# Kernel optimization log

Measured on AMD Instinct MI355X. Metric: run time of the kernel, lower is better.

The kernel has to match this reference:

```python
import jax, jax.numpy as jnp
import numpy as np

U = 359347   # user_num (hardcoded in source)
I = 292589   # item_num (hardcoded in source)
D = 64       # factor_num
NNZ = 4_000_000
B = 32768
LAM = 0.001  # lamada


def setup_inputs() -> dict:
    key = jax.random.key(0)
    ks = jax.random.split(key, 19)
    return {
        "ui_rows": jax.random.randint(ks[0], (NNZ,), 0, U, dtype=jnp.int32),
        "ui_cols": jax.random.randint(ks[1], (NNZ,), 0, I, dtype=jnp.int32),
        "ui_vals": jax.random.uniform(ks[2], (NNZ,), dtype=jnp.float32),
        "iu_vals": jax.random.uniform(ks[3], (NNZ,), dtype=jnp.float32),
        "d_i": jax.random.uniform(ks[4], (U,), dtype=jnp.float32),
        "d_j": jax.random.uniform(ks[5], (I,), dtype=jnp.float32),
        "embed_user": jax.random.normal(ks[6], (U, D), dtype=jnp.float32) * 0.01,
        "embed_item": jax.random.normal(ks[7], (I, D), dtype=jnp.float32) * 0.01,
        "add_w": jax.random.normal(ks[8], (1, 3), dtype=jnp.float32),
        "fw1": jax.random.normal(ks[9], (2 * D, D), dtype=jnp.float32) * (1.0 / np.sqrt(D)),
        "fb1": jax.random.normal(ks[10], (2 * D,), dtype=jnp.float32) * 0.01,
        "fw2": jax.random.normal(ks[11], (D, 2 * D), dtype=jnp.float32) * (1.0 / np.sqrt(2 * D)),
        "fb2": jax.random.normal(ks[12], (D,), dtype=jnp.float32) * 0.01,
        "user_bias": jax.random.normal(ks[13], (U, 1), dtype=jnp.float32) * 0.01,
        "item_bias": jax.random.normal(ks[14], (I, 1), dtype=jnp.float32) * 0.01,
        "avg_rating": jax.random.uniform(ks[15], (1,), dtype=jnp.float32) * 5.0,
        "user0": jax.random.randint(ks[16], (B,), 0, U, dtype=jnp.int32),
        "item_i0": jax.random.randint(ks[17], (B,), 0, I, dtype=jnp.int32),
        "ratings": jax.random.uniform(ks[18], (B,), dtype=jnp.float32) * 5.0,
    }


def _spmm(rows, cols, vals, x, num_rows):
    # sparse [num_rows, *] COO @ dense x : gather rows of x by col index,
    # scale by edge value, scatter-add into destination rows.
    return jax.ops.segment_sum(vals[:, None] * x[cols], rows, num_segments=num_rows)


def _leaky(x):
    return jnp.where(x > 0, x, 0.1 * x)


def _user_filter(x, fw1, fb1, fw2, fb2):
    h = _leaky(x @ fw1.T + fb1)
    return _leaky(h @ fw2.T + fb2)


def reference(ui_rows, ui_cols, ui_vals, iu_vals, d_i, d_j,
              embed_user, embed_item, add_w, fw1, fb1, fw2, fb2,
              user_bias, item_bias, avg_rating, user0, item_i0, ratings):
    ue, ie = embed_user, embed_item
    # layer 1: SpMM + degree-scaled residual + ReLU
    g1_u = jax.nn.relu(_spmm(ui_rows, ui_cols, ui_vals, ie, U) + ue * d_i[:, None])
    g1_i = jax.nn.relu(_spmm(ui_cols, ui_rows, iu_vals, ue, I) + ie * d_j[:, None])
    # layer 2
    g2_u = jax.nn.relu(_spmm(ui_rows, ui_cols, ui_vals, g1_i, U) + g1_u * d_i[:, None])
    g2_i = jax.nn.relu(_spmm(ui_cols, ui_rows, iu_vals, g1_u, I) + g1_i * d_j[:, None])
    # learned combination of the 3 layers: Linear(3,1) over the stacked axis
    w = add_w[0]  # [3]
    gcn_u = w[0] * ue + w[1] * g1_u + w[2] * g2_u   # [U, D]
    gcn_i = w[0] * ie + w[1] * g1_i + w[2] * g2_i   # [I, D]
    # batch lookup + shared filter MLP
    user = _user_filter(gcn_u[user0], fw1, fb1, fw2, fb2)      # [B, D]
    item = _user_filter(gcn_i[item_i0], fw1, fb1, fw2, fb2)    # [B, D]
    pred = (user * item).sum(-1) + user_bias[user0, 0] + item_bias[item_i0, 0] + avg_rating
    l2 = LAM * jnp.mean(gcn_u ** 2) + LAM * jnp.mean(gcn_i ** 2)
    loss2 = jnp.mean((pred - ratings) ** 2)
    return loss2 + l2
```

## Files before the change

### kernel.cpp

```cpp
#include <hip/hip_runtime.h>

#define U_NUM 359347
#define I_NUM 292589
#define DDIM  64
#define NNZ_N 4000000
#define BATCH 32768
#define LAM_F 0.001f
#define ACC_SLOTS 2048

#define EPB   4096
#define NBLK  ((NNZ_N + EPB - 1) / EPB)
#define NB_U  ((U_NUM + 1023) >> 10)
#define NB_I  ((I_NUM + 1023) >> 10)

__device__ __forceinline__ float leaky(float x) { return x > 0.f ? x : 0.1f * x; }

__device__ __forceinline__ unsigned short f2bf(float f) {
    unsigned b = __float_as_uint(f);
    b = (b + 0x7FFF + ((b >> 16) & 1)) >> 16;
    return (unsigned short)b;
}
__device__ __forceinline__ float bf2f(unsigned short u) {
    return __uint_as_float((unsigned)u << 16);
}
__device__ __forceinline__ float bflo(unsigned u) { return __uint_as_float(u << 16); }
__device__ __forceinline__ float bfhi(unsigned u) { return __uint_as_float(u & 0xffff0000u); }

__global__ __launch_bounds__(256) void f2bf_k(
    const float4* __restrict__ in, ushort4* __restrict__ out, size_t n4)
{
    size_t stride = (size_t)gridDim.x * 256;
    for (size_t i = (size_t)blockIdx.x * 256 + threadIdx.x; i < n4; i += stride) {
        float4 v = in[i];
        ushort4 o;
        o.x = f2bf(v.x); o.y = f2bf(v.y); o.z = f2bf(v.z); o.w = f2bf(v.w);
        out[i] = o;
    }
}

__global__ __launch_bounds__(256) void l1hist_k(
    const int* __restrict__ keys, int* __restrict__ gh, int nb)
{
    __shared__ int h[512];
    for (int i = threadIdx.x; i < nb; i += 256) h[i] = 0;
    __syncthreads();
    int base = blockIdx.x * EPB;
    int end = min(base + EPB, NNZ_N);
    for (int e = base + threadIdx.x; e < end; e += 256)
        atomicAdd(&h[keys[e] >> 10], 1);
    __syncthreads();
    for (int i = threadIdx.x; i < nb; i += 256)
        gh[i * NBLK + blockIdx.x] = h[i];
}

__global__ __launch_bounds__(256) void scan1_k(int* __restrict__ a, int n, int* __restrict__ bsum)
{
    __shared__ int s[256];
    int t = threadIdx.x;
    int base = blockIdx.x * 1024 + t * 4;
    int v[4];
#pragma unroll
    for (int j = 0; j < 4; ++j) v[j] = (base + j < n) ? a[base + j] : 0;
    s[t] = v[0] + v[1] + v[2] + v[3];
    __syncthreads();
    for (int off = 1; off < 256; off <<= 1) {
        int x = (t >= off) ? s[t - off] : 0;
        __syncthreads();
        s[t] += x;
        __syncthreads();
    }
    if (t == 255) bsum[blockIdx.x] = s[255];
    int run = (t > 0) ? s[t - 1] : 0;
#pragma unroll
    for (int j = 0; j < 4; ++j) {
        if (base + j < n) a[base + j] = run;
        run += v[j];
    }
}

__global__ __launch_bounds__(512) void scan2_k(int* __restrict__ bsum, int nb)
{
    __shared__ int s[512];
    int t = threadIdx.x;
    int v = (t < nb) ? bsum[t] : 0;
    s[t] = v;
    __syncthreads();
    for (int off = 1; off < 512; off <<= 1) {
        int x = (t >= off) ? s[t - off] : 0;
        __syncthreads();
        s[t] += x;
        __syncthreads();
    }
    if (t < nb) bsum[t] = s[t] - v;
}

__global__ __launch_bounds__(256) void scan3_k(int* __restrict__ a, int n,
                                               const int* __restrict__ bsum)
{
    int add = bsum[blockIdx.x];
    int base = blockIdx.x * 1024 + threadIdx.x * 4;
#pragma unroll
    for (int j = 0; j < 4; ++j)
        if (base + j < n) a[base + j] += add;
}

__global__ __launch_bounds__(256) void l1scatter_k(
    const int* __restrict__ keys, const int* __restrict__ gh, int nb,
    int2* __restrict__ out)
{
    __shared__ int cur[512];
    for (int i = threadIdx.x; i < nb; i += 256) cur[i] = gh[i * NBLK + blockIdx.x];
    __syncthreads();
    int base = blockIdx.x * EPB;
    int end = min(base + EPB, NNZ_N);
    for (int e = base + threadIdx.x; e < end; e += 256) {
        int k = keys[e];
        int pos = atomicAdd(&cur[k >> 10], 1);
        out[pos] = make_int2(k, e);
    }
}

__global__ __launch_bounds__(256) void l2sort_k(
    const int2* __restrict__ tmp, const int* __restrict__ gh, int nb,
    const int* __restrict__ colArr, const float* __restrict__ valArr,
    int* __restrict__ ptr, int nrows, int2* __restrict__ ent)
{
    __shared__ int hist[1024];
    __shared__ int ssc[256];
    int b = blockIdx.x;
    int t = threadIdx.x;
    int bucket_base = gh[b * NBLK];
    int bucket_end  = (b == nb - 1) ? NNZ_N : gh[(b + 1) * NBLK];
    for (int i = t; i < 1024; i += 256) hist[i] = 0;
    __syncthreads();
    for (int e = bucket_base + t; e < bucket_end; e += 256)
        atomicAdd(&hist[tmp[e].x & 1023], 1);
    __syncthreads();
    int v0 = hist[t * 4], v1 = hist[t * 4 + 1], v2 = hist[t * 4 + 2], v3 = hist[t * 4 + 3];
    ssc[t] = v0 + v1 + v2 + v3;
    __syncthreads();
    for (int off = 1; off < 256; off <<= 1) {
        int x = (t >= off) ? ssc[t - off] : 0;
        __syncthreads();
        ssc[t] += x;
        __syncthreads();
    }
    int run = (t > 0) ? ssc[t - 1] : 0;
    int g0 = run, g1 = run + v0, g2 = g1 + v1, g3 = g2 + v2;
    hist[t * 4] = g0; hist[t * 4 + 1] = g1; hist[t * 4 + 2] = g2; hist[t * 4 + 3] = g3;
    int rbase = b << 10;
    if (rbase + t * 4 < nrows)     ptr[rbase + t * 4]     = bucket_base + g0;
    if (rbase + t * 4 + 1 < nrows) ptr[rbase + t * 4 + 1] = bucket_base + g1;
    if (rbase + t * 4 + 2 < nrows) ptr[rbase + t * 4 + 2] = bucket_base + g2;
    if (rbase + t * 4 + 3 < nrows) ptr[rbase + t * 4 + 3] = bucket_base + g3;
    if (b == nb - 1 && t == 0) ptr[nrows] = NNZ_N;
    __syncthreads();
    for (int e = bucket_base + t; e < bucket_end; e += 256) {
        int2 q = tmp[e];
        int pos = bucket_base + atomicAdd(&hist[q.x & 1023], 1);
        ent[pos] = make_int2(colArr[q.y], __float_as_int(valArr[q.y]));
    }
}

template <int MODE>
__global__ __launch_bounds__(256) void spmm_csr_k(
    const int* __restrict__ ptr, const int2* __restrict__ ent,
    const unsigned short* __restrict__ x, const unsigned short* base,
    const float* __restrict__ deg, unsigned short* out, int nrows,
    const unsigned short* __restrict__ embed, const float* __restrict__ add_w,
    float* __restrict__ accArr)
{
    int wv = threadIdx.x >> 6, lane = threadIdx.x & 63;
    int r = blockIdx.x * 4 + wv;
    __shared__ float ssum[4];
    if (r < nrows) {
        int s0 = __builtin_amdgcn_readfirstlane(ptr[r]);
        int e0 = __builtin_amdgcn_readfirstlane(ptr[r + 1]);
        float a0 = 0.f, a1 = 0.f, a2 = 0.f, a3 = 0.f;
        int k = s0;
        for (; k + 4 <= e0; k += 4) {
            int2 q0 = ent[k], q1 = ent[k + 1], q2 = ent[k + 2], q3 = ent[k + 3];
            float x0 = bf2f(x[(size_t)q0.x * DDIM + lane]);
            float x1 = bf2f(x[(size_t)q1.x * DDIM + lane]);
            float x2 = bf2f(x[(size_t)q2.x * DDIM + lane]);
            float x3 = bf2f(x[(size_t)q3.x * DDIM + lane]);
            a0 = fmaf(__int_as_float(q0.y), x0, a0);
            a1 = fmaf(__int_as_float(q1.y), x1, a1);
            a2 = fmaf(__int_as_float(q2.y), x2, a2);
            a3 = fmaf(__int_as_float(q3.y), x3, a3);
        }
        for (; k < e0; ++k) {
            int2 q = ent[k];
            a0 = fmaf(__int_as_float(q.y), bf2f(x[(size_t)q.x * DDIM + lane]), a0);
        }
        float acc = (a0 + a1) + (a2 + a3);
        float bb = bf2f(base[(size_t)r * DDIM + lane]);
        float o = fmaxf(fmaf(bb, deg[r], acc), 0.f);
        if (MODE == 0) {
            out[(size_t)r * DDIM + lane] = f2bf(o);
        } else {
            float g = fmaf(add_w[0], bf2f(embed[(size_t)r * DDIM + lane]),
                           fmaf(add_w[1], bb, add_w[2] * o));
            out[(size_t)r * DDIM + lane] = f2bf(g);
            float sq = g * g;
            for (int off = 32; off; off >>= 1) sq += __shfl_down(sq, off);
            if (lane == 0) ssum[wv] = sq;
        }
    } else if (MODE == 1) {
        if (lane == 0) ssum[wv] = 0.f;
    }
    if (MODE == 1) {
        __syncthreads();
        if (threadIdx.x == 0)
            atomicAdd(&accArr[blockIdx.x & (ACC_SLOTS - 1)],
                      ssum[0] + ssum[1] + ssum[2] + ssum[3]);
    }
}

__global__ __launch_bounds__(256) void mlp_k(
    const int* __restrict__ user0, const int* __restrict__ item0,
    const unsigned short* __restrict__ gcnU, const unsigned short* __restrict__ gcnI,
    const float* __restrict__ fw1, const float* __restrict__ fb1,
    const float* __restrict__ fw2, const float* __restrict__ fb2,
    unsigned short* __restrict__ ou, unsigned short* __restrict__ oi)
{
    __shared__ unsigned short xs[64][72];
    __shared__ unsigned short w1s[128][68];
    __shared__ unsigned short w2s[64][140];
    __shared__ unsigned short hs[128][72];
    __shared__ float b1s[128];
    __shared__ float b2s[64];

    int t = threadIdx.x;
    int side = blockIdx.x >> 9;
    int tile = blockIdx.x & 511;
    const int* sel = side ? item0 : user0;
    const unsigned short* gcn = side ? gcnI : gcnU;
    unsigned short* outp = side ? oi : ou;

    {
        int r = t >> 2, c = t & 3;
        int idx = sel[tile * 64 + r];
        const ushort4* src = (const ushort4*)(gcn + (size_t)idx * 64 + c * 16);
        ushort4 v0 = src[0], v1 = src[1], v2 = src[2], v3 = src[3];
        int k0 = c * 16;
        xs[k0 +  0][r] = v0.x; xs[k0 +  1][r] = v0.y; xs[k0 +  2][r] = v0.z; xs[k0 +  3][r] = v0.w;
        xs[k0 +  4][r] = v1.x; xs[k0 +  5][r] = v1.y; xs[k0 +  6][r] = v1.z; xs[k0 +  7][r] = v1.w;
        xs[k0 +  8][r] = v2.x; xs[k0 +  9][r] = v2.y; xs[k0 + 10][r] = v2.z; xs[k0 + 11][r] = v2.w;
        xs[k0 + 12][r] = v3.x; xs[k0 + 13][r] = v3.y; xs[k0 + 14][r] = v3.z; xs[k0 + 15][r] = v3.w;
    }
#pragma unroll
    for (int i = 0; i < 8; ++i) {
        int flat = i * 1024 + t * 4;
        float4 w = *(const float4*)(fw1 + flat);
        int o = flat >> 6, k = flat & 63;
        *(unsigned*)&w1s[o][k]     = (unsigned)f2bf(w.x) | ((unsigned)f2bf(w.y) << 16);
        *(unsigned*)&w1s[o][k + 2] = (unsigned)f2bf(w.z) | ((unsigned)f2bf(w.w) << 16);
        float4 u = *(const float4*)(fw2 + flat);
        int o2 = flat >> 7, k2 = flat & 127;
        *(unsigned*)&w2s[o2][k2]     = (unsigned)f2bf(u.x) | ((unsigned)f2bf(u.y) << 16);
        *(unsigned*)&w2s[o2][k2 + 2] = (unsigned)f2bf(u.z) | ((unsigned)f2bf(u.w) << 16);
    }
    if (t < 128) b1s[t] = fb1[t];
    if (t < 64)  b2s[t] = fb2[t];
    __syncthreads();

    int sg = t & 15, og = t >> 4;

    float acc[4][8];
#pragma unroll
    for (int i = 0; i < 4; ++i)
#pragma unroll
        for (int j = 0; j < 8; ++j) acc[i][j] = 0.f;

    for (int kc = 0; kc < 64; kc += 4) {
        uint2 xp0 = *(const uint2*)&xs[kc    ][sg * 4];
        uint2 xp1 = *(const uint2*)&xs[kc + 1][sg * 4];
        uint2 xp2 = *(const uint2*)&xs[kc + 2][sg * 4];
        uint2 xp3 = *(const uint2*)&xs[kc + 3][sg * 4];
        float x0[4] = { bflo(xp0.x), bfhi(xp0.x), bflo(xp0.y), bfhi(xp0.y) };
        float x1[4] = { bflo(xp1.x), bfhi(xp1.x), bflo(xp1.y), bfhi(xp1.y) };
        float x2[4] = { bflo(xp2.x), bfhi(xp2.x), bflo(xp2.y), bfhi(xp2.y) };
        float x3[4] = { bflo(xp3.x), bfhi(xp3.x), bflo(xp3.y), bfhi(xp3.y) };
#pragma unroll
        for (int j = 0; j < 8; ++j) {
            uint2 wp = *(const uint2*)&w1s[og * 8 + j][kc];
            float w0 = bflo(wp.x), w1v = bfhi(wp.x), w2v = bflo(wp.y), w3v = bfhi(wp.y);
#pragma unroll
            for (int i = 0; i < 4; ++i) {
                acc[i][j] = fmaf(x0[i], w0,  acc[i][j]);
                acc[i][j] = fmaf(x1[i], w1v, acc[i][j]);
                acc[i][j] = fmaf(x2[i], w2v, acc[i][j]);
                acc[i][j] = fmaf(x3[i], w3v, acc[i][j]);
            }
        }
    }
#pragma unroll
    for (int j = 0; j < 8; ++j) {
        int o = og * 8 + j;
        float b = b1s[o];
        float h0 = leaky(acc[0][j] + b), h1 = leaky(acc[1][j] + b);
        float h2 = leaky(acc[2][j] + b), h3 = leaky(acc[3][j] + b);
        *(unsigned*)&hs[o][sg * 4]     = (unsigned)f2bf(h0) | ((unsigned)f2bf(h1) << 16);
        *(unsigned*)&hs[o][sg * 4 + 2] = (unsigned)f2bf(h2) | ((unsigned)f2bf(h3) << 16);
    }
    __syncthreads();

    float acc2[4][4];
#pragma unroll
    for (int i = 0; i < 4; ++i)
#pragma unroll
        for (int j = 0; j < 4; ++j) acc2[i][j] = 0.f;

    for (int kc = 0; kc < 128; kc += 4) {
        uint2 hp0 = *(const uint2*)&hs[kc    ][sg * 4];
        uint2 hp1 = *(const uint2*)&hs[kc + 1][sg * 4];
        uint2 hp2 = *(const uint2*)&hs[kc + 2][sg * 4];
        uint2 hp3 = *(const uint2*)&hs[kc + 3][sg * 4];
        float h0[4] = { bflo(hp0.x), bfhi(hp0.x), bflo(hp0.y), bfhi(hp0.y) };
        float h1[4] = { bflo(hp1.x), bfhi(hp1.x), bflo(hp1.y), bfhi(hp1.y) };
        float h2[4] = { bflo(hp2.x), bfhi(hp2.x), bflo(hp2.y), bfhi(hp2.y) };
        float h3[4] = { bflo(hp3.x), bfhi(hp3.x), bflo(hp3.y), bfhi(hp3.y) };
#pragma unroll
        for (int j = 0; j < 4; ++j) {
            uint2 wp = *(const uint2*)&w2s[og * 4 + j][kc];
            float w0 = bflo(wp.x), w1v = bfhi(wp.x), w2v = bflo(wp.y), w3v = bfhi(wp.y);
#pragma unroll
            for (int i = 0; i < 4; ++i) {
                acc2[i][j] = fmaf(h0[i], w0,  acc2[i][j]);
                acc2[i][j] = fmaf(h1[i], w1v, acc2[i][j]);
                acc2[i][j] = fmaf(h2[i], w2v, acc2[i][j]);
                acc2[i][j] = fmaf(h3[i], w3v, acc2[i][j]);
            }
        }
    }
#pragma unroll
    for (int i = 0; i < 4; ++i) {
        float o0 = leaky(acc2[i][0] + b2s[og * 4 + 0]);
        float o1 = leaky(acc2[i][1] + b2s[og * 4 + 1]);
        float o2 = leaky(acc2[i][2] + b2s[og * 4 + 2]);
        float o3 = leaky(acc2[i][3] + b2s[og * 4 + 3]);
        uint2 pp;
        pp.x = (unsigned)f2bf(o0) | ((unsigned)f2bf(o1) << 16);
        pp.y = (unsigned)f2bf(o2) | ((unsigned)f2bf(o3) << 16);
        *(uint2*)(outp + ((size_t)(tile * 64 + sg * 4 + i) * 64 + og * 4)) = pp;
    }
}

__global__ __launch_bounds__(256) void dot_sse_k(
    const unsigned short* __restrict__ ou, const unsigned short* __restrict__ oi,
    const int* __restrict__ user0, const int* __restrict__ item0,
    const float* __restrict__ ub, const float* __restrict__ ib,
    const float* __restrict__ avg, const float* __restrict__ ratings,
    float* __restrict__ sse)
{
    int g = blockIdx.x * 256 + threadIdx.x;
    int b = g >> 2, q = g & 3;
    const uint4* pu = (const uint4*)(ou + (size_t)b * 64 + q * 16);
    const uint4* pi = (const uint4*)(oi + (size_t)b * 64 + q * 16);
    uint4 a0 = pu[0], a1 = pu[1];
    uint4 c0 = pi[0], c1 = pi[1];
    float s = 0.f;
#define DOTP(ua, uc) { s = fmaf(bflo(ua), bflo(uc), s); s = fmaf(bfhi(ua), bfhi(uc), s); }
    DOTP(a0.x, c0.x) DOTP(a0.y, c0.y) DOTP(a0.z, c0.z) DOTP(a0.w, c0.w)
    DOTP(a1.x, c1.x) DOTP(a1.y, c1.y) DOTP(a1.z, c1.z) DOTP(a1.w, c1.w)
#undef DOTP
    s += __shfl_xor(s, 1);
    s += __shfl_xor(s, 2);
    float contrib = 0.f;
    if (q == 0) {
        float pred = s + ub[user0[b]] + ib[item0[b]] + avg[0];
        float d = pred - ratings[b];
        contrib = d * d;
    }
    for (int off = 32; off; off >>= 1) contrib += __shfl_down(contrib, off);
    __shared__ float wsum[4];
    int lane = threadIdx.x & 63, wv = threadIdx.x >> 6;
    if (lane == 0) wsum[wv] = contrib;
    __syncthreads();
    if (threadIdx.x == 0)
        atomicAdd(sse, wsum[0] + wsum[1] + wsum[2] + wsum[3]);
}

__global__ __launch_bounds__(256) void finalize2_k(
    const float* __restrict__ accU, const float* __restrict__ accI,
    const float* __restrict__ sse, float* __restrict__ out)
{
    int t = threadIdx.x;
    float su = 0.f, si = 0.f;
    for (int i = t; i < ACC_SLOTS; i += 256) { su += accU[i]; si += accI[i]; }
    for (int off = 32; off; off >>= 1) {
        su += __shfl_down(su, off);
        si += __shfl_down(si, off);
    }
    __shared__ float s[8];
    int wv = t >> 6, lane = t & 63;
    if (lane == 0) { s[wv] = su; s[wv + 4] = si; }
    __syncthreads();
    if (t == 0) {
        float SU = s[0] + s[1] + s[2] + s[3];
        float SI = s[4] + s[5] + s[6] + s[7];
        out[0] = sse[0] / (float)BATCH
               + LAM_F * (SU / (float)((double)U_NUM * 64.0))
               + LAM_F * (SI / (float)((double)I_NUM * 64.0));
    }
}


extern "C" void kernel_launch(void* const* d_in, const int* in_sizes, int n_in,
                              void* d_out, int out_size, void* d_ws, size_t ws_size,
                              hipStream_t stream)
{
    const int*   ui_rows = (const int*)d_in[0];
    const int*   ui_cols = (const int*)d_in[1];
    const float* ui_vals = (const float*)d_in[2];
    const float* iu_vals = (const float*)d_in[3];
    const float* d_i     = (const float*)d_in[4];
    const float* d_j     = (const float*)d_in[5];
    const float* eu      = (const float*)d_in[6];
    const float* ei      = (const float*)d_in[7];
    const float* add_w   = (const float*)d_in[8];
    const float* fw1     = (const float*)d_in[9];
    const float* fb1     = (const float*)d_in[10];
    const float* fw2     = (const float*)d_in[11];
    const float* fb2     = (const float*)d_in[12];
    const float* ub      = (const float*)d_in[13];
    const float* ib      = (const float*)d_in[14];
    const float* avg     = (const float*)d_in[15];
    const int*   user0   = (const int*)d_in[16];
    const int*   item0   = (const int*)d_in[17];
    const float* ratings = (const float*)d_in[18];

    const size_t U64 = (size_t)U_NUM * DDIM;
    const size_t I64 = (size_t)I_NUM * DDIM;

    int2* ent_u = (int2*)d_ws;
    int2* ent_i = ent_u + NNZ_N;
    int2* tmpb  = ent_i + NNZ_N;
    int*  gh    = (int*)(tmpb + NNZ_N);
    int*  bsum  = gh + (size_t)NB_U * NBLK;
    int*  ptr_u = bsum + 512;
    int*  ptr_i = ptr_u + (U_NUM + 1);
    float* accU = (float*)(ptr_i + (I_NUM + 1));
    float* accI = accU + ACC_SLOTS;
    float* sse  = accI + ACC_SLOTS;
    unsigned short* eu_bf   = (unsigned short*)(sse + 4);
    unsigned short* ei_bf   = eu_bf + U64;
    unsigned short* g1u_bf  = ei_bf + I64;
    unsigned short* g1i_bf  = g1u_bf + U64;
    unsigned short* gcnI_bf = g1i_bf + I64;
    unsigned short* ou_bf   = gcnI_bf + I64;
    unsigned short* oi_bf   = ou_bf + (size_t)BATCH * 64;
    (void)ws_size;

    dim3 blk(256);
    int gu = (U_NUM + 3) / 4, gi = (I_NUM + 3) / 4;

    hipMemsetAsync(accU, 0, (2 * ACC_SLOTS + 4) * sizeof(float), stream);

    f2bf_k<<<2048, blk, 0, stream>>>((const float4*)eu, (ushort4*)eu_bf, U64 / 4);
    f2bf_k<<<2048, blk, 0, stream>>>((const float4*)ei, (ushort4*)ei_bf, I64 / 4);

    {
        int n = NB_U * NBLK;
        int nb1 = (n + 1023) / 1024;
        l1hist_k<<<NBLK, blk, 0, stream>>>(ui_rows, gh, NB_U);
        scan1_k<<<nb1, blk, 0, stream>>>(gh, n, bsum);
        scan2_k<<<1, 512, 0, stream>>>(bsum, nb1);
        scan3_k<<<nb1, blk, 0, stream>>>(gh, n, bsum);
        l1scatter_k<<<NBLK, blk, 0, stream>>>(ui_rows, gh, NB_U, tmpb);
        l2sort_k<<<NB_U, blk, 0, stream>>>(tmpb, gh, NB_U, ui_cols, ui_vals,
                                           ptr_u, U_NUM, ent_u);
    }
    {
        int n = NB_I * NBLK;
        int nb1 = (n + 1023) / 1024;
        l1hist_k<<<NBLK, blk, 0, stream>>>(ui_cols, gh, NB_I);
        scan1_k<<<nb1, blk, 0, stream>>>(gh, n, bsum);
        scan2_k<<<1, 512, 0, stream>>>(bsum, nb1);
        scan3_k<<<nb1, blk, 0, stream>>>(gh, n, bsum);
        l1scatter_k<<<NBLK, blk, 0, stream>>>(ui_cols, gh, NB_I, tmpb);
        l2sort_k<<<NB_I, blk, 0, stream>>>(tmpb, gh, NB_I, ui_rows, iu_vals,
                                           ptr_i, I_NUM, ent_i);
    }

    spmm_csr_k<0><<<gu, blk, 0, stream>>>(ptr_u, ent_u, ei_bf, eu_bf, d_i,
                                          g1u_bf, U_NUM, nullptr, nullptr, nullptr);
    spmm_csr_k<0><<<gi, blk, 0, stream>>>(ptr_i, ent_i, eu_bf, ei_bf, d_j,
                                          g1i_bf, I_NUM, nullptr, nullptr, nullptr);
    spmm_csr_k<1><<<gi, blk, 0, stream>>>(ptr_i, ent_i, g1u_bf, g1i_bf, d_j,
                                          gcnI_bf, I_NUM, ei_bf, add_w, accI);
    spmm_csr_k<1><<<gu, blk, 0, stream>>>(ptr_u, ent_u, g1i_bf, g1u_bf, d_i,
                                          g1u_bf, U_NUM, eu_bf, add_w, accU);

    mlp_k<<<1024, blk, 0, stream>>>(user0, item0, g1u_bf, gcnI_bf,
                                    fw1, fb1, fw2, fb2, ou_bf, oi_bf);
    dot_sse_k<<<BATCH * 4 / 256, blk, 0, stream>>>(ou_bf, oi_bf, user0, item0,
                                                   ub, ib, avg, ratings, sse);
    finalize2_k<<<1, blk, 0, stream>>>(accU, accI, sse, (float*)d_out);
}
```

Measured before the change: 1.211 ms.

## Gather SpMM operands from FP8 copies and split edge arrays into col/bf16 val

New measurement: 1.330 ms. 1.1x slower.

```diff
diff --git a/kernel.cpp b/kernel.cpp
--- a/kernel.cpp
+++ b/kernel.cpp
@@ -26,15 +26,33 @@
 __device__ __forceinline__ float bflo(unsigned u) { return __uint_as_float(u << 16); }
 __device__ __forceinline__ float bfhi(unsigned u) { return __uint_as_float(u & 0xffff0000u); }
 
-__global__ __launch_bounds__(256) void f2bf_k(
-    const float4* __restrict__ in, ushort4* __restrict__ out, size_t n4)
+__device__ __forceinline__ unsigned char f2fp8(float v) {
+    v = fminf(fmaxf(v * 64.f, -440.f), 440.f);
+    unsigned b = __float_as_uint(v * 0x1p-120f);
+    unsigned sign = (b >> 24) & 0x80u;
+    unsigned mag = b & 0x7fffffffu;
+    mag += 0x7ffffu + ((mag >> 20) & 1u);
+    return (unsigned char)(sign | ((mag >> 20) & 0x7fu));
+}
+__device__ __forceinline__ float fp82f(unsigned char c) {
+    unsigned u = c;
+    float f = __uint_as_float(((u & 0x80u) << 24) | ((u & 0x7fu) << 20));
+    return f * 0x1p114f;
+}
+
+__global__ __launch_bounds__(256) void f2bf8_k(
+    const float4* __restrict__ in, ushort4* __restrict__ outb,
+    uchar4* __restrict__ out8, size_t n4)
 {
     size_t stride = (size_t)gridDim.x * 256;
     for (size_t i = (size_t)blockIdx.x * 256 + threadIdx.x; i < n4; i += stride) {
         float4 v = in[i];
         ushort4 o;
         o.x = f2bf(v.x); o.y = f2bf(v.y); o.z = f2bf(v.z); o.w = f2bf(v.w);
-        out[i] = o;
+        outb[i] = o;
+        uchar4 p;
+        p.x = f2fp8(v.x); p.y = f2fp8(v.y); p.z = f2fp8(v.z); p.w = f2fp8(v.w);
+        out8[i] = p;
     }
 }
 
@@ -123,7 +141,8 @@
 __global__ __launch_bounds__(256) void l2sort_k(
     const int2* __restrict__ tmp, const int* __restrict__ gh, int nb,
     const int* __restrict__ colArr, const float* __restrict__ valArr,
-    int* __restrict__ ptr, int nrows, int2* __restrict__ ent)
+    int* __restrict__ ptr, int nrows,
+    int* __restrict__ ecol, unsigned short* __restrict__ eval)
 {
     __shared__ int hist[1024];
     __shared__ int ssc[256];
@@ -158,16 +177,19 @@
     for (int e = bucket_base + t; e < bucket_end; e += 256) {
         int2 q = tmp[e];
         int pos = bucket_base + atomicAdd(&hist[q.x & 1023], 1);
-        ent[pos] = make_int2(colArr[q.y], __float_as_int(valArr[q.y]));
+        ecol[pos] = colArr[q.y];
+        eval[pos] = f2bf(valArr[q.y]);
     }
 }
 
 template <int MODE>
 __global__ __launch_bounds__(256) void spmm_csr_k(
-    const int* __restrict__ ptr, const int2* __restrict__ ent,
-    const unsigned short* __restrict__ x, const unsigned short* base,
+    const int* __restrict__ ptr, const int* __restrict__ ecol,
+    const unsigned short* __restrict__ eval,
+    const unsigned char* __restrict__ x8, const unsigned short* base,
     const float* __restrict__ deg, unsigned short* out, int nrows,
-    const unsigned short* __restrict__ embed, const float* __restrict__ add_w,
+    unsigned char* __restrict__ out8,
+    const unsigned short* embed, const float* __restrict__ add_w,
     float* __restrict__ accArr)
 {
     int wv = threadIdx.x >> 6, lane = threadIdx.x & 63;
@@ -179,25 +201,26 @@
         float a0 = 0.f, a1 = 0.f, a2 = 0.f, a3 = 0.f;
         int k = s0;
         for (; k + 4 <= e0; k += 4) {
-            int2 q0 = ent[k], q1 = ent[k + 1], q2 = ent[k + 2], q3 = ent[k + 3];
-            float x0 = bf2f(x[(size_t)q0.x * DDIM + lane]);
-            float x1 = bf2f(x[(size_t)q1.x * DDIM + lane]);
-            float x2 = bf2f(x[(size_t)q2.x * DDIM + lane]);
-            float x3 = bf2f(x[(size_t)q3.x * DDIM + lane]);
-            a0 = fmaf(__int_as_float(q0.y), x0, a0);
-            a1 = fmaf(__int_as_float(q1.y), x1, a1);
-            a2 = fmaf(__int_as_float(q2.y), x2, a2);
-            a3 = fmaf(__int_as_float(q3.y), x3, a3);
+            int c0 = ecol[k], c1 = ecol[k + 1], c2 = ecol[k + 2], c3 = ecol[k + 3];
+            float v0 = bf2f(eval[k]),     v1 = bf2f(eval[k + 1]);
+            float v2 = bf2f(eval[k + 2]), v3 = bf2f(eval[k + 3]);
+            float x0 = fp82f(x8[(size_t)c0 * DDIM + lane]);
+            float x1 = fp82f(x8[(size_t)c1 * DDIM + lane]);
+            float x2 = fp82f(x8[(size_t)c2 * DDIM + lane]);
+            float x3 = fp82f(x8[(size_t)c3 * DDIM + lane]);
+            a0 = fmaf(v0, x0, a0);
+            a1 = fmaf(v1, x1, a1);
+            a2 = fmaf(v2, x2, a2);
+            a3 = fmaf(v3, x3, a3);
         }
-        for (; k < e0; ++k) {
-            int2 q = ent[k];
-            a0 = fmaf(__int_as_float(q.y), bf2f(x[(size_t)q.x * DDIM + lane]), a0);
-        }
+        for (; k < e0; ++k)
+            a0 = fmaf(bf2f(eval[k]), fp82f(x8[(size_t)ecol[k] * DDIM + lane]), a0);
         float acc = (a0 + a1) + (a2 + a3);
         float bb = bf2f(base[(size_t)r * DDIM + lane]);
         float o = fmaxf(fmaf(bb, deg[r], acc), 0.f);
         if (MODE == 0) {
             out[(size_t)r * DDIM + lane] = f2bf(o);
+            out8[(size_t)r * DDIM + lane] = f2fp8(o);
         } else {
             float g = fmaf(add_w[0], bf2f(embed[(size_t)r * DDIM + lane]),
                            fmaf(add_w[1], bb, add_w[2] * o));
@@ -434,9 +457,14 @@
     const size_t U64 = (size_t)U_NUM * DDIM;
     const size_t I64 = (size_t)I_NUM * DDIM;
 
-    int2* ent_u = (int2*)d_ws;
-    int2* ent_i = ent_u + NNZ_N;
-    int2* tmpb  = ent_i + NNZ_N;
+    int*            ecol_u = (int*)d_ws;
+    unsigned short* eval_u = (unsigned short*)(ecol_u + NNZ_N);
+    int*            ecol_i = (int*)(eval_u + NNZ_N);
+    unsigned short* eval_i = (unsigned short*)(ecol_i + NNZ_N);
+    int2* tmpb  = (int2*)(eval_i + NNZ_N);
+    unsigned char*  g1u_f8 = (unsigned char*)tmpb;
+    unsigned short* ou_bf  = (unsigned short*)(g1u_f8 + ((U64 + 15) & ~15ull));
+    unsigned short* oi_bf  = ou_bf + (size_t)BATCH * 64;
     int*  gh    = (int*)(tmpb + NNZ_N);
     int*  bsum  = gh + (size_t)NB_U * NBLK;
     int*  ptr_u = bsum + 512;
@@ -444,13 +472,13 @@
     float* accU = (float*)(ptr_i + (I_NUM + 1));
     float* accI = accU + ACC_SLOTS;
     float* sse  = accI + ACC_SLOTS;
-    unsigned short* eu_bf   = (unsigned short*)(sse + 4);
-    unsigned short* ei_bf   = eu_bf + U64;
-    unsigned short* g1u_bf  = ei_bf + I64;
-    unsigned short* g1i_bf  = g1u_bf + U64;
-    unsigned short* gcnI_bf = g1i_bf + I64;
-    unsigned short* ou_bf   = gcnI_bf + I64;
-    unsigned short* oi_bf   = ou_bf + (size_t)BATCH * 64;
+    unsigned short* eu_bf  = (unsigned short*)(sse + 4);
+    unsigned short* ei_bf  = eu_bf + U64;
+    unsigned short* g1u_bf = ei_bf + I64;
+    unsigned short* g1i_bf = g1u_bf + U64;
+    unsigned char*  eu_f8  = (unsigned char*)(g1i_bf + I64);
+    unsigned char*  ei_f8  = eu_f8 + U64;
+    unsigned char*  g1i_f8 = ei_f8 + I64;
     (void)ws_size;
 
     dim3 blk(256);
@@ -458,8 +486,10 @@
 
     hipMemsetAsync(accU, 0, (2 * ACC_SLOTS + 4) * sizeof(float), stream);
 
-    f2bf_k<<<2048, blk, 0, stream>>>((const float4*)eu, (ushort4*)eu_bf, U64 / 4);
-    f2bf_k<<<2048, blk, 0, stream>>>((const float4*)ei, (ushort4*)ei_bf, I64 / 4);
+    f2bf8_k<<<2048, blk, 0, stream>>>((const float4*)eu, (ushort4*)eu_bf,
+                                      (uchar4*)eu_f8, U64 / 4);
+    f2bf8_k<<<2048, blk, 0, stream>>>((const float4*)ei, (ushort4*)ei_bf,
+                                      (uchar4*)ei_f8, I64 / 4);
 
     {
         int n = NB_U * NBLK;
@@ -470,7 +500,7 @@
         scan3_k<<<nb1, blk, 0, stream>>>(gh, n, bsum);
         l1scatter_k<<<NBLK, blk, 0, stream>>>(ui_rows, gh, NB_U, tmpb);
         l2sort_k<<<NB_U, blk, 0, stream>>>(tmpb, gh, NB_U, ui_cols, ui_vals,
-                                           ptr_u, U_NUM, ent_u);
+                                           ptr_u, U_NUM, ecol_u, eval_u);
     }
     {
         int n = NB_I * NBLK;
@@ -481,19 +511,19 @@
         scan3_k<<<nb1, blk, 0, stream>>>(gh, n, bsum);
         l1scatter_k<<<NBLK, blk, 0, stream>>>(ui_cols, gh, NB_I, tmpb);
         l2sort_k<<<NB_I, blk, 0, stream>>>(tmpb, gh, NB_I, ui_rows, iu_vals,
-                                           ptr_i, I_NUM, ent_i);
-    }
-
-    spmm_csr_k<0><<<gu, blk, 0, stream>>>(ptr_u, ent_u, ei_bf, eu_bf, d_i,
-                                          g1u_bf, U_NUM, nullptr, nullptr, nullptr);
-    spmm_csr_k<0><<<gi, blk, 0, stream>>>(ptr_i, ent_i, eu_bf, ei_bf, d_j,
-                                          g1i_bf, I_NUM, nullptr, nullptr, nullptr);
-    spmm_csr_k<1><<<gi, blk, 0, stream>>>(ptr_i, ent_i, g1u_bf, g1i_bf, d_j,
-                                          gcnI_bf, I_NUM, ei_bf, add_w, accI);
-    spmm_csr_k<1><<<gu, blk, 0, stream>>>(ptr_u, ent_u, g1i_bf, g1u_bf, d_i,
-                                          g1u_bf, U_NUM, eu_bf, add_w, accU);
-
-    mlp_k<<<1024, blk, 0, stream>>>(user0, item0, g1u_bf, gcnI_bf,
+                                           ptr_i, I_NUM, ecol_i, eval_i);
+    }
+
+    spmm_csr_k<0><<<gu, blk, 0, stream>>>(ptr_u, ecol_u, eval_u, ei_f8, eu_bf, d_i,
+                                          g1u_bf, U_NUM, g1u_f8, nullptr, nullptr, nullptr);
+    spmm_csr_k<0><<<gi, blk, 0, stream>>>(ptr_i, ecol_i, eval_i, eu_f8, ei_bf, d_j,
+                                          g1i_bf, I_NUM, g1i_f8, nullptr, nullptr, nullptr);
+    spmm_csr_k<1><<<gi, blk, 0, stream>>>(ptr_i, ecol_i, eval_i, g1u_f8, g1i_bf, d_j,
+                                          ei_bf, I_NUM, nullptr, ei_bf, add_w, accI);
+    spmm_csr_k<1><<<gu, blk, 0, stream>>>(ptr_u, ecol_u, eval_u, g1i_f8, g1u_bf, d_i,
+                                          g1u_bf, U_NUM, nullptr, eu_bf, add_w, accU);
+
+    mlp_k<<<1024, blk, 0, stream>>>(user0, item0, g1u_bf, ei_bf,
                                     fw1, fb1, fw2, fb2, ou_bf, oi_bf);
     dot_sse_k<<<BATCH * 4 / 256, blk, 0, stream>>>(ou_bf, oi_bf, user0, item0,
                                                    ub, ib, avg, ratings, sse);
```
